# Kernel optimization log

Hardware: AMD Instinct MI355X
Metric: run time of the kernel (lower is better)

The kernel has to match this reference:

```python
import jax, jax.numpy as jnp
import numpy as np

B, S, D, H = 2, 2048, 1024, 16
HD = D // H
EPS = 1e-5

def _ln(x, g, b):
    mu = jnp.mean(x, axis=-1, keepdims=True)
    var = jnp.var(x, axis=-1, keepdims=True)
    return (x - mu) * jax.lax.rsqrt(var + EPS) * g + b

def setup_inputs() -> dict:
    key = jax.random.key(0)
    ks = jax.random.split(key, 6)
    sc = lambda n: 1.0 / np.sqrt(n)
    return {
        "x": jax.random.normal(ks[0], (B, S, D), jnp.float32),
        "W_qkv": jax.random.normal(ks[1], (D, 3 * D), jnp.float32) * sc(D),
        "b_qkv": jnp.zeros((3 * D,), jnp.float32),
        "W_o": jax.random.normal(ks[2], (D, D), jnp.float32) * sc(D),
        "b_o": jnp.zeros((D,), jnp.float32),
        "W_fc": jax.random.normal(ks[3], (D, 4 * D), jnp.float32) * sc(D),
        "b_fc": jnp.zeros((4 * D,), jnp.float32),
        "W_pr": jax.random.normal(ks[4], (4 * D, D), jnp.float32) * sc(4 * D),
        "b_pr": jnp.zeros((D,), jnp.float32),
        "g1": jnp.ones((D,), jnp.float32),
        "beta1": jnp.zeros((D,), jnp.float32),
        "g2": jnp.ones((D,), jnp.float32),
        "beta2": jnp.zeros((D,), jnp.float32),
    }

def reference(x, W_qkv, b_qkv, W_o, b_o, W_fc, b_fc, W_pr, b_pr, g1, beta1, g2, beta2):
    # pre-norm attention
    h = _ln(x, g1, beta1)
    qkv = h @ W_qkv + b_qkv                      # [B,S,3D]
    q, k, v = jnp.split(qkv, 3, axis=-1)
    q = q.reshape(B, S, H, HD).transpose(0, 2, 1, 3)  # [B,H,S,hd]
    k = k.reshape(B, S, H, HD).transpose(0, 2, 1, 3)
    v = v.reshape(B, S, H, HD).transpose(0, 2, 1, 3)
    scores = jnp.einsum('bhqd,bhkd->bhqk', q, k) / np.sqrt(HD)
    causal = jnp.tril(jnp.ones((S, S), bool))
    scores = jnp.where(causal, scores, -jnp.inf)
    attn = jax.nn.softmax(scores, axis=-1)
    out = jnp.einsum('bhqk,bhkd->bhqd', attn, v)
    out = out.transpose(0, 2, 1, 3).reshape(B, S, D)
    x = x + out @ W_o + b_o
    # pre-norm MLP (exact erf GELU, matching torch F.gelu default)
    h2 = _ln(x, g2, beta2)
    h2 = jax.nn.gelu(h2 @ W_fc + b_fc, approximate=False)
    x = x + h2 @ W_pr + b_pr
    return x
```

## Files before the change

### kernel.cpp

```cpp
#include <hip/hip_runtime.h>
#include <cstdint>
#include <cstddef>

#define Bb 2
#define Ss 2048
#define Dd 1024
#define Hh 16

typedef __attribute__((ext_vector_type(8))) short short8;
typedef __attribute__((ext_vector_type(4))) short short4v;
typedef __attribute__((ext_vector_type(4))) float float4v;

__device__ inline short f2bf(float f) {
  unsigned u = __builtin_bit_cast(unsigned, f);
  u = (u + 0x7fffu + ((u >> 16) & 1u)) >> 16;
  return (short)u;
}

__device__ inline float bf2f(short s) {
  unsigned u = ((unsigned)(unsigned short)s) << 16;
  return __builtin_bit_cast(float, u);
}

__device__ inline void gl_lds16(const void* g, void* l) {
  __builtin_amdgcn_global_load_lds(
      (__attribute__((address_space(1))) void*)(void*)(g),
      (__attribute__((address_space(3))) void*)(l), 16, 0, 0);
}

#define MFMA(a, b, c) __builtin_amdgcn_mfma_f32_16x16x32_bf16((a), (b), (c), 0, 0, 0)

__device__ __forceinline__ void ln_row(const float* __restrict__ x,
                                       const float* __restrict__ g,
                                       const float* __restrict__ be,
                                       short* __restrict__ out, int row,
                                       float* red) {
  int tid = threadIdx.x;
  const float4* xr = (const float4*)(x + (size_t)row * Dd);
  float4 v = xr[tid];
  float s = v.x + v.y + v.z + v.w;
  float q = v.x * v.x + v.y * v.y + v.z * v.z + v.w * v.w;
#pragma unroll
  for (int off = 1; off < 64; off <<= 1) {
    s += __shfl_xor(s, off);
    q += __shfl_xor(q, off);
  }
  int w = tid >> 6;
  if ((tid & 63) == 0) { red[w] = s; red[4 + w] = q; }
  __syncthreads();
  s = red[0] + red[1] + red[2] + red[3];
  q = red[4] + red[5] + red[6] + red[7];
  float mu = s * (1.0f / Dd);
  float var = q * (1.0f / Dd) - mu * mu;
  float rstd = rsqrtf(var + 1e-5f);
  float4 gv = ((const float4*)g)[tid], bv = ((const float4*)be)[tid];
  short4v o;
  o.x = f2bf((v.x - mu) * rstd * gv.x + bv.x);
  o.y = f2bf((v.y - mu) * rstd * gv.y + bv.y);
  o.z = f2bf((v.z - mu) * rstd * gv.z + bv.z);
  o.w = f2bf((v.w - mu) * rstd * gv.w + bv.w);
  *(short4v*)(out + (size_t)row * Dd + tid * 4) = o;
}

__global__ __launch_bounds__(256) void prep_kernel(
    const float* __restrict__ W0, short* __restrict__ T0,
    const float* __restrict__ W1, short* __restrict__ T1,
    const float* __restrict__ W2, short* __restrict__ T2,
    const float* __restrict__ W3, short* __restrict__ T3,
    const float* __restrict__ x, const float* __restrict__ g1,
    const float* __restrict__ be1, short* __restrict__ h1) {
  __shared__ __align__(16) float t[32][33];
  int id = blockIdx.x;
  if (id >= 12288) {
    ln_row(x, g1, be1, h1, id - 12288, &t[0][0]);
    return;
  }
  const float* W; short* Wt; int N, K, tix;
  if (id < 3072)      { W = W0; Wt = T0; N = 3072; K = 1024; tix = id; }
  else if (id < 4096) { W = W1; Wt = T1; N = 1024; K = 1024; tix = id - 3072; }
  else if (id < 8192) { W = W2; Wt = T2; N = 4096; K = 1024; tix = id - 4096; }
  else                { W = W3; Wt = T3; N = 1024; K = 4096; tix = id - 8192; }
  int nx = N / 32;
  int n0 = (tix % nx) * 32, k0 = (tix / nx) * 32;
  int tx = threadIdx.x & 31, ty = threadIdx.x >> 5;
#pragma unroll
  for (int i = 0; i < 4; i++)
    t[ty + 8 * i][tx] = W[(size_t)(k0 + ty + 8 * i) * N + n0 + tx];
  __syncthreads();
#pragma unroll
  for (int i = 0; i < 4; i++)
    Wt[(size_t)(n0 + ty + 8 * i) * K + k0 + tx] = f2bf(t[tx][ty + 8 * i]);
}

__global__ __launch_bounds__(256) void reduce_ln_kernel(const float* __restrict__ x,
                                                        const float* __restrict__ bias,
                                                        const short* __restrict__ parts,
                                                        const float* __restrict__ g,
                                                        const float* __restrict__ be,
                                                        float* __restrict__ x1,
                                                        short* __restrict__ h2) {
  int row = blockIdx.x, tid = threadIdx.x;
  size_t base = (size_t)row * Dd + tid * 4;
  float4 v = *(const float4*)(x + base);
  float4 bv = ((const float4*)bias)[tid];
  v.x += bv.x; v.y += bv.y; v.z += bv.z; v.w += bv.w;
#pragma unroll
  for (int s = 0; s < 2; s++) {
    short4v p = *(const short4v*)(parts + (size_t)s * 4096 * Dd + base);
    v.x += bf2f(p.x); v.y += bf2f(p.y); v.z += bf2f(p.z); v.w += bf2f(p.w);
  }
  *(float4*)(x1 + base) = v;
  float s = v.x + v.y + v.z + v.w;
  float q = v.x * v.x + v.y * v.y + v.z * v.z + v.w * v.w;
#pragma unroll
  for (int off = 1; off < 64; off <<= 1) {
    s += __shfl_xor(s, off);
    q += __shfl_xor(q, off);
  }
  __shared__ float as_[4], aq_[4];
  int w = tid >> 6;
  if ((tid & 63) == 0) { as_[w] = s; aq_[w] = q; }
  __syncthreads();
  s = as_[0] + as_[1] + as_[2] + as_[3];
  q = aq_[0] + aq_[1] + aq_[2] + aq_[3];
  float mu = s * (1.0f / Dd);
  float var = q * (1.0f / Dd) - mu * mu;
  float rstd = rsqrtf(var + 1e-5f);
  float4 gv = ((const float4*)g)[tid], b2 = ((const float4*)be)[tid];
  short4v o;
  o.x = f2bf((v.x - mu) * rstd * gv.x + b2.x);
  o.y = f2bf((v.y - mu) * rstd * gv.y + b2.y);
  o.z = f2bf((v.z - mu) * rstd * gv.z + b2.z);
  o.w = f2bf((v.w - mu) * rstd * gv.w + b2.w);
  *(short4v*)(h2 + base) = o;
}

__global__ __launch_bounds__(256) void reduce_kernel(const float* __restrict__ src,
                                                     const float* __restrict__ bias,
                                                     const short* __restrict__ parts,
                                                     float* __restrict__ dst) {
  int row = blockIdx.x, tid = threadIdx.x;
  size_t base = (size_t)row * Dd + tid * 4;
  float4 v = *(const float4*)(src + base);
  float4 bv = ((const float4*)bias)[tid];
  v.x += bv.x; v.y += bv.y; v.z += bv.z; v.w += bv.w;
#pragma unroll
  for (int s = 0; s < 2; s++) {
    short4v p = *(const short4v*)(parts + (size_t)s * 4096 * Dd + base);
    v.x += bf2f(p.x); v.y += bf2f(p.y); v.z += bf2f(p.z); v.w += bf2f(p.w);
  }
  *(float4*)(dst + base) = v;
}

template <int MODE>
__device__ __forceinline__ void gemm_tile(const short* __restrict__ A,
                                          const short* __restrict__ Bt,
                                          const float* __restrict__ bias,
                                          void* __restrict__ outp,
                                          short* __restrict__ vtp,
                                          int M, int N, int K,
                                          int m0, int n0, int zp,
                                          int ks, int ke, char* smem) {
  short* As = (short*)smem;
  short* Bs = (short*)smem + 128 * 64;
  const int tid = threadIdx.x;
  const int w = tid >> 6, lane = tid & 63;
  const int sr = lane >> 3;
  const int sc = lane & 7;
  const int gc = sc ^ sr;
  const int fr = lane & 15;
  const int g = lane >> 4;
  const int wm = (w >> 1) * 64, wn = (w & 1) * 64;
  float4v acc[4][4] = {};
  const short* Ag = A + (size_t)(m0 + w * 32 + sr) * K + gc * 8;
  const short* Bg = Bt + (size_t)(n0 + w * 32 + sr) * K + gc * 8;
  short* Asw = As + (w * 32 + sr) * 64 + sc * 8;
  short* Bsw = Bs + (w * 32 + sr) * 64 + sc * 8;
#pragma unroll
  for (int i = 0; i < 4; i++) {
    gl_lds16(Ag + (size_t)(i * 8) * K + ks, Asw + i * 8 * 64);
    gl_lds16(Bg + (size_t)(i * 8) * K + ks, Bsw + i * 8 * 64);
  }
  for (int k0 = ks; k0 < ke; k0 += 64) {
    __syncthreads();
    short8 a[2][4], b[2][4];
#pragma unroll
    for (int kh = 0; kh < 2; kh++) {
#pragma unroll
      for (int i = 0; i < 4; i++) {
        int row = wm + i * 16 + fr;
        int slot = (g + kh * 4) ^ (row & 7);
        a[kh][i] = *(const short8*)(As + row * 64 + slot * 8);
      }
#pragma unroll
      for (int j = 0; j < 4; j++) {
        int row = wn + j * 16 + fr;
        int slot = (g + kh * 4) ^ (row & 7);
        b[kh][j] = *(const short8*)(Bs + row * 64 + slot * 8);
      }
    }
    __syncthreads();
    if (k0 + 64 < ke) {
#pragma unroll
      for (int i = 0; i < 4; i++) {
        gl_lds16(Ag + (size_t)(i * 8) * K + k0 + 64, Asw + i * 8 * 64);
        gl_lds16(Bg + (size_t)(i * 8) * K + k0 + 64, Bsw + i * 8 * 64);
      }
    }
#pragma unroll
    for (int kh = 0; kh < 2; kh++)
#pragma unroll
      for (int i = 0; i < 4; i++)
#pragma unroll
        for (int j = 0; j < 4; j++)
          acc[kh & 0 ? 0 : i][j] = MFMA(a[kh][i], b[kh][j], acc[i][j]);
  }
  const int crow = g * 4;
  const int ccol = fr;
#pragma unroll
  for (int i = 0; i < 4; i++) {
#pragma unroll
    for (int j = 0; j < 4; j++) {
      int col = n0 + wn + j * 16 + ccol;
      float bcol = (MODE == 3) ? 0.f : bias[col];
      short sh[4];
#pragma unroll
      for (int r = 0; r < 4; r++) {
        int row = m0 + wm + i * 16 + crow + r;
        float v = acc[i][j][r] + bcol;
        if (MODE == 4) {
          sh[r] = f2bf(v);
          ((short*)outp)[(size_t)row * N + col] = sh[r];
        } else if (MODE == 2) {
          float y = 0.79788456f * (v + 0.044715f * v * v * v);
          float e = __builtin_amdgcn_exp2f(y * 2.885390082f);
          float th = 1.0f - 2.0f * __builtin_amdgcn_rcpf(e + 1.0f);
          v = 0.5f * v * (1.0f + th);
          ((short*)outp)[(size_t)row * N + col] = f2bf(v);
        } else {
          short* pp = (short*)outp + (size_t)zp * M * N;
          pp[(size_t)row * N + col] = f2bf(v);
        }
      }
      if (MODE == 4 && col >= 2048) {
        int hd = col - 2048;
        int rbase = m0 + wm + i * 16 + crow;
        int bq = rbase >> 11, sb = rbase & 2047;
        int bh = bq * 16 + (hd >> 6), d = hd & 63;
        short4v pk;
        pk.x = sh[0]; pk.y = sh[1]; pk.z = sh[2]; pk.w = sh[3];
        *(short4v*)(vtp + (size_t)(bh * 64 + d) * Ss + sb) = pk;
      }
    }
  }
}

__global__ __launch_bounds__(256) void k_gemm_qkv(const short* __restrict__ A,
                                                  const short* __restrict__ Bt,
                                                  const float* __restrict__ bias,
                                                  short* __restrict__ o,
                                                  short* __restrict__ Vt) {
  __shared__ __align__(16) char smem[32768];
  int t = blockIdx.x;
  int c8 = t & 7, tt = t >> 3;
  int m0 = ((c8 >> 1) * 8 + tt / 12) * 128;
  int n0 = ((c8 & 1) * 12 + tt % 12) * 128;
  gemm_tile<4>(A, Bt, bias, o, Vt, 4096, 3072, 1024, m0, n0, 0, 0, 1024, smem);
}

__global__ __launch_bounds__(256) void k_gemm_fc(const short* __restrict__ A,
                                                 const short* __restrict__ Bt,
                                                 const float* __restrict__ bias,
                                                 short* __restrict__ o) {
  __shared__ __align__(16) char smem[32768];
  int t = blockIdx.x;
  int c8 = t & 7, tt = t >> 3;
  int m0 = ((c8 >> 1) * 8 + tt / 16) * 128;
  int n0 = ((c8 & 1) * 16 + tt % 16) * 128;
  gemm_tile<2>(A, Bt, bias, o, nullptr, 4096, 4096, 1024, m0, n0, 0, 0, 1024, smem);
}

__global__ __launch_bounds__(256) void k_gemm_wo(const short* __restrict__ A,
                                                 const short* __restrict__ Bt,
                                                 short* __restrict__ parts) {
  __shared__ __align__(16) char smem[32768];
  int c = blockIdx.x;
  int z = c >> 8, rem = c & 255;
  int c8 = rem & 7, tt = rem >> 3;
  int m0 = (c8 * 4 + tt / 8) * 128, n0 = (tt % 8) * 128;
  gemm_tile<3>(A, Bt, nullptr, parts, nullptr, 4096, 1024, 1024, m0, n0, z,
               z * 512, z * 512 + 512, smem);
}

__global__ __launch_bounds__(256) void k_gemm_pr(const short* __restrict__ A,
                                                 const short* __restrict__ Bt,
                                                 short* __restrict__ parts) {
  __shared__ __align__(16) char smem[32768];
  int c = blockIdx.x;
  int z = c >> 8, rem = c & 255;
  int c8 = rem & 7, tt = rem >> 3;
  int m0 = (c8 * 4 + tt / 8) * 128, n0 = (tt % 8) * 128;
  gemm_tile<3>(A, Bt, nullptr, parts, nullptr, 4096, 1024, 4096, m0, n0, z,
               z * 2048, z * 2048 + 2048, smem);
}

__global__ __launch_bounds__(256) void flash_kernel(const short* __restrict__ qkv,
                                                    const short* __restrict__ Vt,
                                                    short* __restrict__ att) {
  __shared__ __align__(16) short Ks[4096];
  __shared__ __align__(16) short Vs[4096];
  __shared__ __align__(16) short P[4][16 * 72];
  const int w = threadIdx.x >> 6, lane = threadIdx.x & 63;
  const int qb = 31 - (blockIdx.x >> 5);
  const int bh = blockIdx.x & 31;
  const int b = bh >> 4, h = bh & 15;
  const int qbase = qb * 64 + w * 16;
  const int q = lane & 15;
  const int g = lane >> 4;
  const int fk = g * 8;
  short* Pw = &P[w][0];

  const int L0 = w * 64 + lane, L1 = L0 + 256;
  const int r0 = L0 >> 3, c0 = (L0 & 7) ^ (r0 & 7);
  const int r1 = L1 >> 3, c1 = (L1 & 7) ^ (r1 & 7);
  const short* kg0 = qkv + (size_t)(b * Ss + r0) * 3072 + 1024 + h * 64 + c0 * 8;
  const short* kg1 = qkv + (size_t)(b * Ss + r1) * 3072 + 1024 + h * 64 + c1 * 8;
  const short* vg0 = Vt + (size_t)(bh * 64 + r0) * Ss + c0 * 8;
  const short* vg1 = Vt + (size_t)(bh * 64 + r1) * Ss + c1 * 8;

  short8 qf[2];
  {
    const short* qrow = qkv + (size_t)(b * Ss + qbase + q) * 3072 + h * 64;
    qf[0] = *(const short8*)(qrow + fk);
    qf[1] = *(const short8*)(qrow + 32 + fk);
  }
  float4v o[4] = {};
  float l_i = 0.f;
  const float sc = 0.125f * 1.44269504088896f;
  const int nkt = qb + 1;

  gl_lds16(kg0, Ks + L0 * 8);
  gl_lds16(kg1, Ks + L1 * 8);
  gl_lds16(vg0, Vs + L0 * 8);
  gl_lds16(vg1, Vs + L1 * 8);

  for (int kt = 0; kt < nkt; kt++) {
    const int kbase = kt * 64;
    __syncthreads();

    short8 kf[4][2], vf[4][2];
#pragma unroll
    for (int t = 0; t < 4; t++) {
      const int row = 16 * t + q;
      const int sw = (g ^ (row & 7)) * 8;
      kf[t][0] = *(const short8*)(Ks + row * 64 + sw);
      kf[t][1] = *(const short8*)(Ks + row * 64 + (sw ^ 32));
      vf[t][0] = *(const short8*)(Vs + row * 64 + sw);
      vf[t][1] = *(const short8*)(Vs + row * 64 + (sw ^ 32));
    }
    __syncthreads();
    if (kt + 1 < nkt) {
      const size_t nb = (size_t)(kbase + 64);
      gl_lds16(kg0 + nb * 3072, Ks + L0 * 8);
      gl_lds16(kg1 + nb * 3072, Ks + L1 * 8);
      gl_lds16(vg0 + nb, Vs + L0 * 8);
      gl_lds16(vg1 + nb, Vs + L1 * 8);
    }

    float4v s[4] = {};
#pragma unroll
    for (int t = 0; t < 4; t++) {
      s[t] = MFMA(kf[t][0], qf[0], s[t]);
      s[t] = MFMA(kf[t][1], qf[1], s[t]);
    }
    const bool maskt = (kbase + 63 > qbase);
    const int qlim = qbase + q - kbase;
    float p[4][4];
    float rs = 0.f;
#pragma unroll
    for (int t = 0; t < 4; t++) {
#pragma unroll
      for (int r = 0; r < 4; r++) {
        float v = s[t][r] * sc;
        if (maskt && (16 * t + 4 * g + r > qlim)) v = -3.0e38f;
        float e = __builtin_amdgcn_exp2f(v);
        p[t][r] = e;
        rs += e;
      }
    }
    rs += __shfl_xor(rs, 16);
    rs += __shfl_xor(rs, 32);
    l_i += rs;
#pragma unroll
    for (int t = 0; t < 4; t++) {
      unsigned lo = (unsigned)(unsigned short)f2bf(p[t][0]) |
                    ((unsigned)(unsigned short)f2bf(p[t][1]) << 16);
      unsigned hi = (unsigned)(unsigned short)f2bf(p[t][2]) |
                    ((unsigned)(unsigned short)f2bf(p[t][3]) << 16);
      uint2 u; u.x = lo; u.y = hi;
      *(uint2*)(Pw + q * 72 + 16 * t + 4 * g) = u;
    }
    asm volatile("s_waitcnt lgkmcnt(0)" ::: "memory");
    short8 pb0 = *(const short8*)(Pw + q * 72 + fk);
    short8 pb1 = *(const short8*)(Pw + q * 72 + 32 + fk);
#pragma unroll
    for (int t = 0; t < 4; t++) {
      o[t] = MFMA(vf[t][0], pb0, o[t]);
      o[t] = MFMA(vf[t][1], pb1, o[t]);
    }
  }
  const float inv = 1.0f / l_i;
  const int orow = b * Ss + qbase + q;
#pragma unroll
  for (int t = 0; t < 4; t++) {
    short4v ov;
    ov.x = f2bf(o[t][0] * inv);
    ov.y = f2bf(o[t][1] * inv);
    ov.z = f2bf(o[t][2] * inv);
    ov.w = f2bf(o[t][3] * inv);
    *(short4v*)(att + (size_t)orow * Dd + h * 64 + 16 * t + 4 * g) = ov;
  }
}

extern "C" void kernel_launch(void* const* d_in, const int* in_sizes, int n_in,
                              void* d_out, int out_size, void* d_ws, size_t ws_size,
                              hipStream_t stream) {
  const float* x    = (const float*)d_in[0];
  const float* Wqkv = (const float*)d_in[1];
  const float* bqkv = (const float*)d_in[2];
  const float* Wo   = (const float*)d_in[3];
  const float* bo   = (const float*)d_in[4];
  const float* Wfc  = (const float*)d_in[5];
  const float* bfc  = (const float*)d_in[6];
  const float* Wpr  = (const float*)d_in[7];
  const float* bpr  = (const float*)d_in[8];
  const float* g1   = (const float*)d_in[9];
  const float* be1  = (const float*)d_in[10];
  const float* g2   = (const float*)d_in[11];
  const float* be2  = (const float*)d_in[12];

  char* ws = (char*)d_ws;
  const size_t MB = 1024 * 1024;
  short* h1     = (short*)(ws + 0);
  short* qkvb   = (short*)(ws + 8 * MB);
  short* partWo = (short*)(ws + 0);
  short* partPr = (short*)(ws + 0);
  short* Vt     = (short*)(ws + 32 * MB);
  short* att    = (short*)(ws + 40 * MB);
  float* x1     = (float*)(ws + 48 * MB);
  short* h2     = (short*)(ws + 64 * MB);
  short* geluo  = (short*)(ws + 72 * MB);
  short* WtQkv  = (short*)(ws + 104 * MB);
  short* WtO    = (short*)(ws + 110 * MB);
  short* WtFc   = (short*)(ws + 112 * MB);
  short* WtPr   = (short*)(ws + 120 * MB);

  prep_kernel<<<16384, 256, 0, stream>>>(Wqkv, WtQkv, Wo, WtO, Wfc, WtFc,
                                         Wpr, WtPr, x, g1, be1, h1);
  k_gemm_qkv<<<768, 256, 0, stream>>>(h1, WtQkv, bqkv, qkvb, Vt);
  flash_kernel<<<1024, 256, 0, stream>>>(qkvb, Vt, att);
  k_gemm_wo<<<512, 256, 0, stream>>>(att, WtO, partWo);
  reduce_ln_kernel<<<4096, 256, 0, stream>>>(x, bo, partWo, g2, be2, x1, h2);
  k_gemm_fc<<<1024, 256, 0, stream>>>(h2, WtFc, bfc, geluo);
  k_gemm_pr<<<512, 256, 0, stream>>>(geluo, WtPr, partPr);
  reduce_kernel<<<4096, 256, 0, stream>>>(x1, bpr, partPr, (float*)d_out);
}
```

Before: 309.4 us.

## Replace 128x128 GEMM tiles with 256x256 double-buffered 8-wave ping-pong kernel

```diff
diff --git a/kernel.cpp b/kernel.cpp
--- a/kernel.cpp
+++ b/kernel.cpp
@@ -105,7 +105,7 @@
   float4 bv = ((const float4*)bias)[tid];
   v.x += bv.x; v.y += bv.y; v.z += bv.z; v.w += bv.w;
 #pragma unroll
-  for (int s = 0; s < 2; s++) {
+  for (int s = 0; s < 4; s++) {
     short4v p = *(const short4v*)(parts + (size_t)s * 4096 * Dd + base);
     v.x += bf2f(p.x); v.y += bf2f(p.y); v.z += bf2f(p.z); v.w += bf2f(p.w);
   }
@@ -145,7 +145,7 @@
   float4 bv = ((const float4*)bias)[tid];
   v.x += bv.x; v.y += bv.y; v.z += bv.z; v.w += bv.w;
 #pragma unroll
-  for (int s = 0; s < 2; s++) {
+  for (int s = 0; s < 4; s++) {
     short4v p = *(const short4v*)(parts + (size_t)s * 4096 * Dd + base);
     v.x += bf2f(p.x); v.y += bf2f(p.y); v.z += bf2f(p.z); v.w += bf2f(p.w);
   }
@@ -153,80 +153,148 @@
 }
 
 template <int MODE>
-__device__ __forceinline__ void gemm_tile(const short* __restrict__ A,
-                                          const short* __restrict__ Bt,
-                                          const float* __restrict__ bias,
-                                          void* __restrict__ outp,
-                                          short* __restrict__ vtp,
-                                          int M, int N, int K,
-                                          int m0, int n0, int zp,
-                                          int ks, int ke, char* smem) {
-  short* As = (short*)smem;
-  short* Bs = (short*)smem + 128 * 64;
+__device__ __forceinline__ void gemm256(const short* __restrict__ A,
+                                        const short* __restrict__ Bt,
+                                        const float* __restrict__ bias,
+                                        void* __restrict__ outp,
+                                        short* __restrict__ vtp,
+                                        int M, int N, int K,
+                                        int m0, int n0, int zp,
+                                        int ks, int nt, char* smem) {
   const int tid = threadIdx.x;
-  const int w = tid >> 6, lane = tid & 63;
-  const int sr = lane >> 3;
-  const int sc = lane & 7;
-  const int gc = sc ^ sr;
-  const int fr = lane & 15;
-  const int g = lane >> 4;
-  const int wm = (w >> 1) * 64, wn = (w & 1) * 64;
-  float4v acc[4][4] = {};
-  const short* Ag = A + (size_t)(m0 + w * 32 + sr) * K + gc * 8;
-  const short* Bg = Bt + (size_t)(n0 + w * 32 + sr) * K + gc * 8;
-  short* Asw = As + (w * 32 + sr) * 64 + sc * 8;
-  short* Bsw = Bs + (w * 32 + sr) * 64 + sc * 8;
-#pragma unroll
-  for (int i = 0; i < 4; i++) {
-    gl_lds16(Ag + (size_t)(i * 8) * K + ks, Asw + i * 8 * 64);
-    gl_lds16(Bg + (size_t)(i * 8) * K + ks, Bsw + i * 8 * 64);
-  }
-  for (int k0 = ks; k0 < ke; k0 += 64) {
-    __syncthreads();
-    short8 a[2][4], b[2][4];
-#pragma unroll
-    for (int kh = 0; kh < 2; kh++) {
-#pragma unroll
-      for (int i = 0; i < 4; i++) {
-        int row = wm + i * 16 + fr;
-        int slot = (g + kh * 4) ^ (row & 7);
-        a[kh][i] = *(const short8*)(As + row * 64 + slot * 8);
-      }
-#pragma unroll
-      for (int j = 0; j < 4; j++) {
-        int row = wn + j * 16 + fr;
-        int slot = (g + kh * 4) ^ (row & 7);
-        b[kh][j] = *(const short8*)(Bs + row * 64 + slot * 8);
-      }
-    }
-    __syncthreads();
-    if (k0 + 64 < ke) {
-#pragma unroll
-      for (int i = 0; i < 4; i++) {
-        gl_lds16(Ag + (size_t)(i * 8) * K + k0 + 64, Asw + i * 8 * 64);
-        gl_lds16(Bg + (size_t)(i * 8) * K + k0 + 64, Bsw + i * 8 * 64);
-      }
-    }
-#pragma unroll
-    for (int kh = 0; kh < 2; kh++)
-#pragma unroll
-      for (int i = 0; i < 4; i++)
-#pragma unroll
-        for (int j = 0; j < 4; j++)
-          acc[kh & 0 ? 0 : i][j] = MFMA(a[kh][i], b[kh][j], acc[i][j]);
-  }
+  const int wid = tid >> 6, lane = tid & 63;
+  const int wm = wid >> 2, wn = wid & 3;
+  const int fr = lane & 15, g = lane >> 4;
+  const int r0 = tid >> 3, sl = tid & 7;
+  const int gcs = sl ^ (r0 & 7);
+  const int lOff = r0 * 128 + sl * 16;
+
+  const short* gA = A + (size_t)(m0 + r0) * K + ks + gcs * 8;
+  const short* gB = Bt + (size_t)(n0 + r0) * K + ks + gcs * 8;
+
+  auto stageA = [&](int t) {
+    char* la = smem + (t & 1) * 65536 + lOff;
+    const short* ga = gA + t * 64;
+#pragma unroll
+    for (int i = 0; i < 4; i++)
+      gl_lds16(ga + (size_t)(64 * i) * K, la + i * 8192);
+  };
+  auto stageB = [&](int t) {
+    char* lb = smem + (t & 1) * 65536 + 32768 + lOff;
+    const short* gb = gB + t * 64;
+#pragma unroll
+    for (int i = 0; i < 4; i++)
+      gl_lds16(gb + (size_t)(64 * i) * K, lb + i * 8192);
+  };
+
+  const int aoff0 = (g ^ (fr & 7)) * 16;
+  const int aoff1 = ((g + 4) ^ (fr & 7)) * 16;
+  const int arow = (wm * 128 + fr) * 128;
+  const int brow = (wn * 64 + fr) * 128;
+
+  float4v acc[8][4] = {};
+  short8 a[4][2], b[4][2];
+
+  stageA(0);
+  stageB(0);
+  if (nt > 1) {
+    stageA(1);
+    asm volatile("s_waitcnt vmcnt(4)" ::: "memory");
+  } else {
+    asm volatile("s_waitcnt vmcnt(0)" ::: "memory");
+  }
+  __builtin_amdgcn_s_barrier();
+
+  for (int t = 0; t < nt; t++) {
+    char* lA = smem + (t & 1) * 65536;
+    char* lB = lA + 32768;
+#pragma unroll
+    for (int i = 0; i < 4; i++) {
+      a[i][0] = *(const short8*)(lA + arow + i * 2048 + aoff0);
+      a[i][1] = *(const short8*)(lA + arow + i * 2048 + aoff1);
+    }
+    if (t + 1 < nt) stageB(t + 1);
+#pragma unroll
+    for (int j = 0; j < 2; j++) {
+      b[j][0] = *(const short8*)(lB + brow + j * 2048 + aoff0);
+      b[j][1] = *(const short8*)(lB + brow + j * 2048 + aoff1);
+    }
+    __builtin_amdgcn_s_barrier();
+    asm volatile("s_waitcnt lgkmcnt(0)" ::: "memory");
+    __builtin_amdgcn_s_setprio(1);
+#pragma unroll
+    for (int i = 0; i < 4; i++)
+#pragma unroll
+      for (int j = 0; j < 2; j++) {
+        acc[i][j] = MFMA(a[i][0], b[j][0], acc[i][j]);
+        acc[i][j] = MFMA(a[i][1], b[j][1], acc[i][j]);
+      }
+    __builtin_amdgcn_s_setprio(0);
+    __builtin_amdgcn_s_barrier();
+#pragma unroll
+    for (int j = 2; j < 4; j++) {
+      b[j][0] = *(const short8*)(lB + brow + j * 2048 + aoff0);
+      b[j][1] = *(const short8*)(lB + brow + j * 2048 + aoff1);
+    }
+    __builtin_amdgcn_s_barrier();
+    asm volatile("s_waitcnt lgkmcnt(0)" ::: "memory");
+    __builtin_amdgcn_s_setprio(1);
+#pragma unroll
+    for (int i = 0; i < 4; i++)
+#pragma unroll
+      for (int j = 2; j < 4; j++) {
+        acc[i][j] = MFMA(a[i][0], b[j][0], acc[i][j]);
+        acc[i][j] = MFMA(a[i][1], b[j][1], acc[i][j]);
+      }
+    __builtin_amdgcn_s_setprio(0);
+    __builtin_amdgcn_s_barrier();
+#pragma unroll
+    for (int i = 0; i < 4; i++) {
+      a[i][0] = *(const short8*)(lA + arow + 8192 + i * 2048 + aoff0);
+      a[i][1] = *(const short8*)(lA + arow + 8192 + i * 2048 + aoff1);
+    }
+    __builtin_amdgcn_s_barrier();
+    asm volatile("s_waitcnt lgkmcnt(0)" ::: "memory");
+    __builtin_amdgcn_s_setprio(1);
+#pragma unroll
+    for (int i = 0; i < 4; i++)
+#pragma unroll
+      for (int j = 2; j < 4; j++) {
+        acc[4 + i][j] = MFMA(a[i][0], b[j][0], acc[4 + i][j]);
+        acc[4 + i][j] = MFMA(a[i][1], b[j][1], acc[4 + i][j]);
+      }
+    __builtin_amdgcn_s_setprio(0);
+    __builtin_amdgcn_s_barrier();
+    if (t + 2 < nt) stageA(t + 2);
+    __builtin_amdgcn_s_setprio(1);
+#pragma unroll
+    for (int i = 0; i < 4; i++)
+#pragma unroll
+      for (int j = 0; j < 2; j++) {
+        acc[4 + i][j] = MFMA(a[i][0], b[j][0], acc[4 + i][j]);
+        acc[4 + i][j] = MFMA(a[i][1], b[j][1], acc[4 + i][j]);
+      }
+    __builtin_amdgcn_s_setprio(0);
+    if (t + 1 < nt) {
+      if (t + 2 < nt)
+        asm volatile("s_waitcnt vmcnt(4)" ::: "memory");
+      else
+        asm volatile("s_waitcnt vmcnt(0)" ::: "memory");
+      __builtin_amdgcn_s_barrier();
+    }
+  }
+
   const int crow = g * 4;
-  const int ccol = fr;
-#pragma unroll
-  for (int i = 0; i < 4; i++) {
+#pragma unroll
+  for (int i = 0; i < 8; i++) {
 #pragma unroll
     for (int j = 0; j < 4; j++) {
-      int col = n0 + wn + j * 16 + ccol;
+      int col = n0 + wn * 64 + j * 16 + fr;
       float bcol = (MODE == 3) ? 0.f : bias[col];
       short sh[4];
 #pragma unroll
       for (int r = 0; r < 4; r++) {
-        int row = m0 + wm + i * 16 + crow + r;
+        int row = m0 + wm * 128 + i * 16 + crow + r;
         float v = acc[i][j][r] + bcol;
         if (MODE == 4) {
           sh[r] = f2bf(v);
@@ -244,7 +312,7 @@
       }
       if (MODE == 4 && col >= 2048) {
         int hd = col - 2048;
-        int rbase = m0 + wm + i * 16 + crow;
+        int rbase = m0 + wm * 128 + i * 16 + crow;
         int bq = rbase >> 11, sb = rbase & 2047;
         int bh = bq * 16 + (hd >> 6), d = hd & 63;
         short4v pk;
@@ -255,53 +323,51 @@
   }
 }
 
-__global__ __launch_bounds__(256) void k_gemm_qkv(const short* __restrict__ A,
-                                                  const short* __restrict__ Bt,
-                                                  const float* __restrict__ bias,
-                                                  short* __restrict__ o,
-                                                  short* __restrict__ Vt) {
-  __shared__ __align__(16) char smem[32768];
-  int t = blockIdx.x;
-  int c8 = t & 7, tt = t >> 3;
-  int m0 = ((c8 >> 1) * 8 + tt / 12) * 128;
-  int n0 = ((c8 & 1) * 12 + tt % 12) * 128;
-  gemm_tile<4>(A, Bt, bias, o, Vt, 4096, 3072, 1024, m0, n0, 0, 0, 1024, smem);
-}
-
-__global__ __launch_bounds__(256) void k_gemm_fc(const short* __restrict__ A,
-                                                 const short* __restrict__ Bt,
-                                                 const float* __restrict__ bias,
-                                                 short* __restrict__ o) {
-  __shared__ __align__(16) char smem[32768];
-  int t = blockIdx.x;
-  int c8 = t & 7, tt = t >> 3;
-  int m0 = ((c8 >> 1) * 8 + tt / 16) * 128;
-  int n0 = ((c8 & 1) * 16 + tt % 16) * 128;
-  gemm_tile<2>(A, Bt, bias, o, nullptr, 4096, 4096, 1024, m0, n0, 0, 0, 1024, smem);
-}
-
-__global__ __launch_bounds__(256) void k_gemm_wo(const short* __restrict__ A,
-                                                 const short* __restrict__ Bt,
-                                                 short* __restrict__ parts) {
-  __shared__ __align__(16) char smem[32768];
-  int c = blockIdx.x;
-  int z = c >> 8, rem = c & 255;
-  int c8 = rem & 7, tt = rem >> 3;
-  int m0 = (c8 * 4 + tt / 8) * 128, n0 = (tt % 8) * 128;
-  gemm_tile<3>(A, Bt, nullptr, parts, nullptr, 4096, 1024, 1024, m0, n0, z,
-               z * 512, z * 512 + 512, smem);
-}
-
-__global__ __launch_bounds__(256) void k_gemm_pr(const short* __restrict__ A,
-                                                 const short* __restrict__ Bt,
-                                                 short* __restrict__ parts) {
-  __shared__ __align__(16) char smem[32768];
-  int c = blockIdx.x;
-  int z = c >> 8, rem = c & 255;
-  int c8 = rem & 7, tt = rem >> 3;
-  int m0 = (c8 * 4 + tt / 8) * 128, n0 = (tt % 8) * 128;
-  gemm_tile<3>(A, Bt, nullptr, parts, nullptr, 4096, 1024, 4096, m0, n0, z,
-               z * 2048, z * 2048 + 2048, smem);
+__global__ __launch_bounds__(512, 2) void k_gemm_qkv(const short* __restrict__ A,
+                                                     const short* __restrict__ Bt,
+                                                     const float* __restrict__ bias,
+                                                     short* __restrict__ o,
+                                                     short* __restrict__ Vt) {
+  extern __shared__ char smem[];
+  int xcd = blockIdx.x & 7, u = blockIdx.x >> 3;
+  int m0 = ((xcd >> 1) * 4 + u / 6) * 256;
+  int n0 = ((xcd & 1) * 6 + u % 6) * 256;
+  gemm256<4>(A, Bt, bias, o, Vt, 4096, 3072, 1024, m0, n0, 0, 0, 16, smem);
+}
+
+__global__ __launch_bounds__(512, 2) void k_gemm_fc(const short* __restrict__ A,
+                                                    const short* __restrict__ Bt,
+                                                    const float* __restrict__ bias,
+                                                    short* __restrict__ o) {
+  extern __shared__ char smem[];
+  int xcd = blockIdx.x & 7, u = blockIdx.x >> 3;
+  int m0 = ((xcd >> 1) * 4 + (u >> 3)) * 256;
+  int n0 = ((xcd & 1) * 8 + (u & 7)) * 256;
+  gemm256<2>(A, Bt, bias, o, nullptr, 4096, 4096, 1024, m0, n0, 0, 0, 16, smem);
+}
+
+__global__ __launch_bounds__(512, 2) void k_gemm_wo(const short* __restrict__ A,
+                                                    const short* __restrict__ Bt,
+                                                    short* __restrict__ parts) {
+  extern __shared__ char smem[];
+  int xcd = blockIdx.x & 7, u = blockIdx.x >> 3;
+  int z = u >> 3;
+  int m0 = (xcd * 2 + ((u >> 2) & 1)) * 256;
+  int n0 = (u & 3) * 256;
+  gemm256<3>(A, Bt, nullptr, parts, nullptr, 4096, 1024, 1024, m0, n0, z,
+             z * 256, 4, smem);
+}
+
+__global__ __launch_bounds__(512, 2) void k_gemm_pr(const short* __restrict__ A,
+                                                    const short* __restrict__ Bt,
+                                                    short* __restrict__ parts) {
+  extern __shared__ char smem[];
+  int xcd = blockIdx.x & 7, u = blockIdx.x >> 3;
+  int z = u >> 3;
+  int m0 = (xcd * 2 + ((u >> 2) & 1)) * 256;
+  int n0 = (u & 3) * 256;
+  gemm256<3>(A, Bt, nullptr, parts, nullptr, 4096, 1024, 4096, m0, n0, z,
+             z * 1024, 16, smem);
 }
 
 __global__ __launch_bounds__(256) void flash_kernel(const short* __restrict__ qkv,
@@ -457,11 +523,11 @@
 
   prep_kernel<<<16384, 256, 0, stream>>>(Wqkv, WtQkv, Wo, WtO, Wfc, WtFc,
                                          Wpr, WtPr, x, g1, be1, h1);
-  k_gemm_qkv<<<768, 256, 0, stream>>>(h1, WtQkv, bqkv, qkvb, Vt);
+  k_gemm_qkv<<<192, 512, 131072, stream>>>(h1, WtQkv, bqkv, qkvb, Vt);
   flash_kernel<<<1024, 256, 0, stream>>>(qkvb, Vt, att);
-  k_gemm_wo<<<512, 256, 0, stream>>>(att, WtO, partWo);
+  k_gemm_wo<<<256, 512, 131072, stream>>>(att, WtO, partWo);
   reduce_ln_kernel<<<4096, 256, 0, stream>>>(x, bo, partWo, g2, be2, x1, h2);
-  k_gemm_fc<<<1024, 256, 0, stream>>>(h2, WtFc, bfc, geluo);
-  k_gemm_pr<<<512, 256, 0, stream>>>(geluo, WtPr, partPr);
+  k_gemm_fc<<<256, 512, 131072, stream>>>(h2, WtFc, bfc, geluo);
+  k_gemm_pr<<<256, 512, 131072, stream>>>(geluo, WtPr, partPr);
   reduce_kernel<<<4096, 256, 0, stream>>>(x1, bpr, partPr, (float*)d_out);
 }
```

Result: no change. 311.5 us (+0.7%).
